# Optimization experiments

Hardware: AMD Instinct MI355X
Metric: run time of the kernel (lower is better)

The kernel has to match this reference:

```python
import jax, jax.numpy as jnp
import numpy as np

N = 100000
E = 1600000
F = 128
COMP_RATIO = 4
K = max(1, N // COMP_RATIO)


def mean_agg(x, src, tgt, n):
    # mean over in-neighbors: h_i = mean_{(j->i) in edges} x_j
    s = jax.ops.segment_sum(x[src], tgt, num_segments=n)          # [N, F]
    cnt = jax.ops.segment_sum(jnp.ones(src.shape[0], x.dtype), tgt, num_segments=n)
    return s / jnp.maximum(cnt, 1.0)[:, None]


def setup_inputs() -> dict:
    key = jax.random.key(0)
    ks = jax.random.split(key, 10)
    sc = 1.0 / np.sqrt(F)
    return {
        "x": jax.random.normal(ks[0], (N, F), jnp.float32),
        "src": jax.random.randint(ks[1], (E,), 0, N, jnp.int32),
        "tgt": jax.random.randint(ks[2], (E,), 0, N, jnp.int32),
        "W_self": jax.random.normal(ks[3], (F, F), jnp.float32) * sc,
        "W_neigh": jax.random.normal(ks[4], (F, F), jnp.float32) * sc,
        "b_pack": jnp.zeros((F,), jnp.float32),
        "w_score": jax.random.normal(ks[5], (F, 1), jnp.float32) * sc,
        "b_score": jnp.zeros((1,), jnp.float32),
        "W_u1": jax.random.normal(ks[6], (F, F), jnp.float32) * sc,
        "b_u1": jnp.zeros((F,), jnp.float32),
        "W_u2": jax.random.normal(ks[7], (F, F), jnp.float32) * sc,
        "b_u2": jnp.zeros((F,), jnp.float32),
    }


def reference(x, src, tgt, W_self, W_neigh, b_pack, w_score, b_score,
              W_u1, b_u1, W_u2, b_u2):
    # ---- compress ----
    # SAGEConv (mean aggregator): fc_self(x) + fc_neigh(mean_neigh(x)) + bias
    h = x @ W_self + mean_agg(x, src, tgt, N) @ W_neigh + b_pack  # [N, F]
    # scorer: Linear(F,1) + Sigmoid
    score = jax.nn.sigmoid(h @ w_score + b_score)[:, 0]           # [N]
    # pool: topk scores, gate selected features by their score
    sel_scores, idx = jax.lax.top_k(score, K)                     # [K], [K]
    new_val = h[idx] * sel_scores[:, None]                        # [K, F]
    # ---- decompress ----
    z = jnp.zeros((N, F), x.dtype).at[idx].set(new_val)
    # diffusion layer 1 (SageConvExt update_func='diffuse'):
    # propagate neighbor mean, keep the received (seed) features fixed
    d = mean_agg(z, src, tgt, N) @ W_u1 + b_u1
    d = d.at[idx].set(z[idx])
    d = jax.nn.relu(d)
    # diffusion layer 2
    out = mean_agg(d, src, tgt, N) @ W_u2 + b_u2
    out = out.at[idx].set(d[idx])
    return out
```

## Files before the change

### kernel.cpp

```cpp
#include <hip/hip_runtime.h>

#define NN 100000
#define NE 1600000
#define FF 128
#define KK 25000
#define NB ((NN + 255) / 256)
#define BM 64
#define BK 32
#define GEMM_GRID ((NN + BM - 1) / BM)

#define BKT_SHIFT 11
#define NPBK (1 << BKT_SHIFT)
#define NBKT2 ((NN + NPBK - 1) >> BKT_SHIFT)
#define NBLKA 512
#define CHUNKA ((NE + NBLKA - 1) / NBLKA)

__device__ __forceinline__ unsigned short f2b(float f) {
  unsigned u = __float_as_uint(f);
  u += 0x7FFFu + ((u >> 16) & 1u);
  return (unsigned short)(u >> 16);
}
__device__ __forceinline__ unsigned pack2(float lo, float hi) {
  return (unsigned)f2b(lo) | ((unsigned)f2b(hi) << 16);
}

__device__ __forceinline__ unsigned long long topk_key(float s, unsigned i) {
  return (((unsigned long long)__float_as_uint(s)) << 32) |
         (unsigned long long)(0xFFFFFFFFu - i);
}

__global__ __launch_bounds__(256) void k_histA(const int* __restrict__ tgt,
                                               int* __restrict__ histg) {
  __shared__ int h[NBKT2];
  for (int i = threadIdx.x; i < NBKT2; i += 256) h[i] = 0;
  __syncthreads();
  int b = blockIdx.x;
  int e0 = b * CHUNKA, e1 = min(e0 + CHUNKA, NE);
  for (int e = e0 + threadIdx.x; e < e1; e += 256)
    atomicAdd(&h[tgt[e] >> BKT_SHIFT], 1);
  __syncthreads();
  for (int i = threadIdx.x; i < NBKT2; i += 256) histg[i * NBLKA + b] = h[i];
}

__global__ __launch_bounds__(1024) void k_scanA(int* __restrict__ histg,
                                                int* __restrict__ bbase) {
  const int M = NBKT2 * NBLKA;
  const int C = (M + 1023) / 1024;
  __shared__ int part[1024];
  __shared__ int tmp[1024];
  int t = threadIdx.x;
  int i0 = t * C;
  int iend = min(i0 + C, M);
  int s = 0;
  for (int i = i0; i < iend; ++i) s += histg[i];
  part[t] = s;
  __syncthreads();
  int* A = part;
  int* B = tmp;
  for (int off = 1; off < 1024; off <<= 1) {
    int v = A[t] + (t >= off ? A[t - off] : 0);
    B[t] = v;
    __syncthreads();
    int* sw = A; A = B; B = sw;
  }
  int run = (t > 0) ? A[t - 1] : 0;
  for (int i = i0; i < iend; ++i) {
    int v = histg[i];
    histg[i] = run;
    run += v;
  }
  __syncthreads();
  if (t < NBKT2) bbase[t] = histg[t * NBLKA];
  if (t == 0) bbase[NBKT2] = NE;
}

__global__ __launch_bounds__(256) void k_scatterA(const int* __restrict__ src,
                                                  const int* __restrict__ tgt,
                                                  const int* __restrict__ histg,
                                                  int2* __restrict__ pairs) {
  __shared__ int cur[NBKT2];
  int b = blockIdx.x;
  for (int i = threadIdx.x; i < NBKT2; i += 256) cur[i] = histg[i * NBLKA + b];
  __syncthreads();
  int e0 = b * CHUNKA, e1 = min(e0 + CHUNKA, NE);
  for (int e = e0 + threadIdx.x; e < e1; e += 256) {
    int t = tgt[e];
    int p = atomicAdd(&cur[t >> BKT_SHIFT], 1);
    pairs[p] = make_int2(t, src[e]);
  }
}

__global__ __launch_bounds__(1024) void k_bucketB(const int2* __restrict__ pairs,
                                                  const int* __restrict__ bbase,
                                                  int* __restrict__ offsets,
                                                  int* __restrict__ csr) {
  __shared__ int cnt[NPBK];
  __shared__ int part[1024];
  __shared__ int tmp[1024];
  int b = blockIdx.x;
  int t = threadIdx.x;
  int lo = b << BKT_SHIFT;
  int nloc = min(NPBK, NN - lo);
  int base = bbase[b];
  int cntE = bbase[b + 1] - base;
  cnt[t] = 0;
  cnt[t + 1024] = 0;
  __syncthreads();
  for (int p = t; p < cntE; p += 1024)
    atomicAdd(&cnt[pairs[base + p].x - lo], 1);
  __syncthreads();
  int a0 = cnt[2 * t];
  int a1 = cnt[2 * t + 1];
  part[t] = a0 + a1;
  __syncthreads();
  int* A = part;
  int* B = tmp;
  for (int off = 1; off < 1024; off <<= 1) {
    int v = A[t] + (t >= off ? A[t - off] : 0);
    B[t] = v;
    __syncthreads();
    int* sw = A; A = B; B = sw;
  }
  int o0 = (t > 0) ? A[t - 1] : 0;
  int o1 = o0 + a0;
  if (2 * t < nloc) offsets[lo + 2 * t] = base + o0;
  if (2 * t + 1 < nloc) offsets[lo + 2 * t + 1] = base + o1;
  __syncthreads();
  cnt[2 * t] = o0;
  cnt[2 * t + 1] = o1;
  __syncthreads();
  for (int p = t; p < cntE; p += 1024) {
    int2 ts = pairs[base + p];
    int l = ts.x - lo;
    int pos = atomicAdd(&cnt[l], 1);
    csr[base + pos] = ts.y;
  }
  if (b == NBKT2 - 1 && t == 0) offsets[NN] = NE;
}

__global__ __launch_bounds__(256) void k_agg(const float* __restrict__ vals,
                                             const int* __restrict__ csr,
                                             const int* __restrict__ offsets,
                                             float* __restrict__ outv) {
  int w = threadIdx.x >> 6;
  int lane = threadIdx.x & 63;
  int half = lane >> 5;
  int li = lane & 31;
  int node = blockIdx.x * 4 + w;
  if (node >= NN) return;
  int beg = offsets[node];
  int end = offsets[node + 1];
  int deg = end - beg;
  float a0 = 0.f, a1 = 0.f, a2 = 0.f, a3 = 0.f;
  int e = beg;
  int e8 = beg + (deg & ~7);
  for (; e < e8; e += 8) {
    float4 v[4];
#pragma unroll
    for (int q = 0; q < 4; ++q) {
      int j = csr[e + 2 * q + half];
      v[q] = *reinterpret_cast<const float4*>(&vals[(size_t)j * FF + li * 4]);
    }
#pragma unroll
    for (int q = 0; q < 4; ++q) {
      a0 += v[q].x; a1 += v[q].y; a2 += v[q].z; a3 += v[q].w;
    }
  }
  for (; e + 2 <= end; e += 2) {
    int j = csr[e + half];
    float4 v = *reinterpret_cast<const float4*>(&vals[(size_t)j * FF + li * 4]);
    a0 += v.x; a1 += v.y; a2 += v.z; a3 += v.w;
  }
  if (e < end && half == 0) {
    int j = csr[e];
    float4 v = *reinterpret_cast<const float4*>(&vals[(size_t)j * FF + li * 4]);
    a0 += v.x; a1 += v.y; a2 += v.z; a3 += v.w;
  }
  a0 += __shfl_xor(a0, 32, 64);
  a1 += __shfl_xor(a1, 32, 64);
  a2 += __shfl_xor(a2, 32, 64);
  a3 += __shfl_xor(a3, 32, 64);
  if (half == 0) {
    float inv = 1.0f / (float)(deg > 0 ? deg : 1);
    *reinterpret_cast<float4*>(&outv[(size_t)node * FF + li * 4]) =
        make_float4(a0 * inv, a1 * inv, a2 * inv, a3 * inv);
  }
}

template <bool GATED>
__global__ __launch_bounds__(256) void k_agg_bf(const unsigned* __restrict__ vals,
                                                const int* __restrict__ csr,
                                                const int* __restrict__ offsets,
                                                const float* __restrict__ sel,
                                                unsigned* __restrict__ outv) {
  int w = threadIdx.x >> 6;
  int lane = threadIdx.x & 63;
  int half = lane >> 5;
  int li = lane & 31;
  int node = blockIdx.x * 4 + w;
  if (node >= NN) return;
  int beg = offsets[node];
  int end = offsets[node + 1];
  int deg = end - beg;
  float a0 = 0.f, a1 = 0.f, a2 = 0.f, a3 = 0.f;
  int e = beg;
  int e8 = beg + (deg & ~7);
  for (; e < e8; e += 8) {
    uint2 u[4];
#pragma unroll
    for (int q = 0; q < 4; ++q) {
      int j = csr[e + 2 * q + half];
      u[q] = (!GATED || sel[j] != 0.f)
                 ? *reinterpret_cast<const uint2*>(&vals[(size_t)j * (FF / 2) + li * 2])
                 : make_uint2(0u, 0u);
    }
#pragma unroll
    for (int q = 0; q < 4; ++q) {
      a0 += __uint_as_float(u[q].x << 16);
      a1 += __uint_as_float(u[q].x & 0xFFFF0000u);
      a2 += __uint_as_float(u[q].y << 16);
      a3 += __uint_as_float(u[q].y & 0xFFFF0000u);
    }
  }
  for (; e + 2 <= end; e += 2) {
    int j = csr[e + half];
    uint2 u = (!GATED || sel[j] != 0.f)
                  ? *reinterpret_cast<const uint2*>(&vals[(size_t)j * (FF / 2) + li * 2])
                  : make_uint2(0u, 0u);
    a0 += __uint_as_float(u.x << 16);
    a1 += __uint_as_float(u.x & 0xFFFF0000u);
    a2 += __uint_as_float(u.y << 16);
    a3 += __uint_as_float(u.y & 0xFFFF0000u);
  }
  if (e < end && half == 0) {
    int j = csr[e];
    uint2 u = (!GATED || sel[j] != 0.f)
                  ? *reinterpret_cast<const uint2*>(&vals[(size_t)j * (FF / 2) + li * 2])
                  : make_uint2(0u, 0u);
    a0 += __uint_as_float(u.x << 16);
    a1 += __uint_as_float(u.x & 0xFFFF0000u);
    a2 += __uint_as_float(u.y << 16);
    a3 += __uint_as_float(u.y & 0xFFFF0000u);
  }
  a0 += __shfl_xor(a0, 32, 64);
  a1 += __shfl_xor(a1, 32, 64);
  a2 += __shfl_xor(a2, 32, 64);
  a3 += __shfl_xor(a3, 32, 64);
  if (half == 0) {
    float inv = 1.0f / (float)(deg > 0 ? deg : 1);
    uint2 o;
    o.x = pack2(a0 * inv, a1 * inv);
    o.y = pack2(a2 * inv, a3 * inv);
    *reinterpret_cast<uint2*>(&outv[(size_t)node * (FF / 2) + li * 2]) = o;
  }
}

template <int EPI, bool DUAL, bool ABF16>
__global__ __launch_bounds__(256) void k_gemm4(const void* __restrict__ Araw,
                                               const float* __restrict__ W,
                                               const float* __restrict__ A2,
                                               const float* __restrict__ W2,
                                               const float* __restrict__ bias,
                                               const float* __restrict__ aux,
                                               const float* __restrict__ score,
                                               const float* __restrict__ sel,
                                               float* __restrict__ outv,
                                               unsigned* __restrict__ obf,
                                               const float* __restrict__ wsc,
                                               const float* __restrict__ bsc,
                                               float* __restrict__ score_out) {
  __shared__ float As[BK][BM + 4];
  __shared__ float Ws[BK][FF];
  const int tid = threadIdx.x;
  const int tx = tid & 15;
  const int ty = tid >> 4;
  const int m0 = blockIdx.x * BM;

  float acc[4][8];
#pragma unroll
  for (int r = 0; r < 4; ++r)
#pragma unroll
    for (int j = 0; j < 8; ++j) acc[r][j] = 0.f;

  const int NPASS = DUAL ? 2 : 1;
  for (int pass = 0; pass < NPASS; ++pass) {
    const float* Wp = (pass == 0) ? W : W2;
    for (int kt = 0; kt < FF; kt += BK) {
      __syncthreads();
      if (pass == 0 && ABF16) {
        const unsigned* Ab = (const unsigned*)Araw;
#pragma unroll
        for (int t = 0; t < 4; ++t) {
          int i = tid + t * 256;
          int row = i >> 4;
          int cu = i & 15;
          int gr = m0 + row;
          unsigned u = (gr < NN) ? Ab[(size_t)gr * (FF / 2) + (kt >> 1) + cu] : 0u;
          As[cu * 2 + 0][row] = __uint_as_float(u << 16);
          As[cu * 2 + 1][row] = __uint_as_float(u & 0xFFFF0000u);
        }
      } else {
        const float* Ag = (pass == 0) ? (const float*)Araw : A2;
#pragma unroll
        for (int t = 0; t < 2; ++t) {
          int i = tid + t * 256;
          int row = i >> 3;
          int c8 = i & 7;
          int gr = m0 + row;
          float4 v = make_float4(0.f, 0.f, 0.f, 0.f);
          if (gr < NN) v = *(const float4*)&Ag[(size_t)gr * FF + kt + c8 * 4];
          As[c8 * 4 + 0][row] = v.x;
          As[c8 * 4 + 1][row] = v.y;
          As[c8 * 4 + 2][row] = v.z;
          As[c8 * 4 + 3][row] = v.w;
        }
      }
#pragma unroll
      for (int t = 0; t < 4; ++t) {
        int i = tid + t * 256;
        int kr = i >> 5;
        int c4 = i & 31;
        *(float4*)&Ws[kr][c4 * 4] =
            *(const float4*)&Wp[(size_t)(kt + kr) * FF + c4 * 4];
      }
      __syncthreads();
#pragma unroll
      for (int k = 0; k < BK; ++k) {
        float4 a = *(const float4*)&As[k][ty * 4];
        float4 w0 = *(const float4*)&Ws[k][tx * 4];
        float4 w1 = *(const float4*)&Ws[k][tx * 4 + 64];
        float av[4] = {a.x, a.y, a.z, a.w};
        float wv[8] = {w0.x, w0.y, w0.z, w0.w, w1.x, w1.y, w1.z, w1.w};
#pragma unroll
        for (int r = 0; r < 4; ++r)
#pragma unroll
          for (int j = 0; j < 8; ++j) acc[r][j] = fmaf(av[r], wv[j], acc[r][j]);
      }
    }
  }

  float4 b0 = *(const float4*)&bias[tx * 4];
  float4 b1 = *(const float4*)&bias[tx * 4 + 64];
  float bs[8] = {b0.x, b0.y, b0.z, b0.w, b1.x, b1.y, b1.z, b1.w};

  if constexpr (EPI == 0) {
    __shared__ float sp[BM][17];
    float4 s0 = *(const float4*)&wsc[tx * 4];
    float4 s1 = *(const float4*)&wsc[tx * 4 + 64];
    float sv[8] = {s0.x, s0.y, s0.z, s0.w, s1.x, s1.y, s1.z, s1.w};
#pragma unroll
    for (int r = 0; r < 4; ++r) {
      int gi = m0 + ty * 4 + r;
      if (gi >= NN) continue;
      size_t base = (size_t)gi * FF;
      float v[8];
      float p = 0.f;
#pragma unroll
      for (int j = 0; j < 8; ++j) {
        v[j] = acc[r][j] + bs[j];
        p = fmaf(v[j], sv[j], p);
      }
      sp[ty * 4 + r][tx] = p;
      *(float4*)&outv[base + tx * 4] = make_float4(v[0], v[1], v[2], v[3]);
      *(float4*)&outv[base + tx * 4 + 64] = make_float4(v[4], v[5], v[6], v[7]);
    }
    __syncthreads();
    if (tid < BM) {
      int gi = m0 + tid;
      if (gi < NN) {
        float s = 0.f;
#pragma unroll
        for (int t = 0; t < 16; ++t) s += sp[tid][t];
        float z = s + bsc[0];
        score_out[gi] = 1.0f / (1.0f + expf(-z));
      }
    }
  } else {
#pragma unroll
    for (int r = 0; r < 4; ++r) {
      int gi = m0 + ty * 4 + r;
      if (gi >= NN) continue;
      size_t base = (size_t)gi * FF;
      float se = sel[gi];
      if (EPI == 1) {
        float v[8];
        if (se != 0.f) {
          float sc = score[gi];
          float4 x0 = *(const float4*)&aux[base + tx * 4];
          float4 x1 = *(const float4*)&aux[base + tx * 4 + 64];
          float av[8] = {x0.x, x0.y, x0.z, x0.w, x1.x, x1.y, x1.z, x1.w};
#pragma unroll
          for (int j = 0; j < 8; ++j) v[j] = fmaxf(av[j] * sc, 0.f);
          *(float4*)&outv[base + tx * 4] = make_float4(v[0], v[1], v[2], v[3]);
          *(float4*)&outv[base + tx * 4 + 64] = make_float4(v[4], v[5], v[6], v[7]);
        } else {
#pragma unroll
          for (int j = 0; j < 8; ++j) v[j] = fmaxf(acc[r][j] + bs[j], 0.f);
        }
        uint2 p0, p1;
        p0.x = pack2(v[0], v[1]);
        p0.y = pack2(v[2], v[3]);
        p1.x = pack2(v[4], v[5]);
        p1.y = pack2(v[6], v[7]);
        *(uint2*)&obf[(size_t)gi * (FF / 2) + tx * 2] = p0;
        *(uint2*)&obf[(size_t)gi * (FF / 2) + 32 + tx * 2] = p1;
      } else {
        float v[8];
        if (se != 0.f) {
          float4 x0 = *(const float4*)&aux[base + tx * 4];
          float4 x1 = *(const float4*)&aux[base + tx * 4 + 64];
          v[0] = x0.x; v[1] = x0.y; v[2] = x0.z; v[3] = x0.w;
          v[4] = x1.x; v[5] = x1.y; v[6] = x1.z; v[7] = x1.w;
        } else {
#pragma unroll
          for (int j = 0; j < 8; ++j) v[j] = acc[r][j] + bs[j];
        }
        *(float4*)&outv[base + tx * 4] = make_float4(v[0], v[1], v[2], v[3]);
        *(float4*)&outv[base + tx * 4 + 64] = make_float4(v[4], v[5], v[6], v[7]);
      }
    }
  }
}

__global__ void k_init_state(unsigned* state) {
  state[0] = 0u;
  state[1] = 0u;
  state[2] = KK;
}

__global__ __launch_bounds__(256) void k_hist(const float* __restrict__ score,
                                              const unsigned* __restrict__ state,
                                              unsigned* __restrict__ hist,
                                              int bits_fixed) {
  __shared__ unsigned lh[256];
  for (int i = threadIdx.x; i < 256; i += 256) lh[i] = 0;
  __syncthreads();
  unsigned long long prefix =
      (((unsigned long long)state[0]) << 32) | (unsigned long long)state[1];
  int i = blockIdx.x * 256 + threadIdx.x;
  if (i < NN) {
    unsigned long long key = topk_key(score[i], (unsigned)i);
    bool ok = (bits_fixed == 0) ? true : (((key ^ prefix) >> (64 - bits_fixed)) == 0ull);
    if (ok) {
      unsigned b = (unsigned)((key >> (56 - bits_fixed)) & 0xFFull);
      atomicAdd(&lh[b], 1u);
    }
  }
  __syncthreads();
  for (int i2 = threadIdx.x; i2 < 256; i2 += 256)
    if (lh[i2]) atomicAdd(&hist[i2], lh[i2]);
}

__global__ __launch_bounds__(256) void k_select_round(unsigned* __restrict__ state,
                                                      unsigned* __restrict__ hist,
                                                      int bits_fixed) {
  __shared__ unsigned h[256];
  int t = threadIdx.x;
  h[t] = hist[t];
  hist[t] = 0;
  __syncthreads();
  if (t == 0) {
    unsigned rem = state[2];
    unsigned long long prefix =
        (((unsigned long long)state[0]) << 32) | (unsigned long long)state[1];
    unsigned cum = 0;
    int bstar = 0;
    for (int b = 255; b >= 0; --b) {
      unsigned c = h[b];
      if (cum + c >= rem) { bstar = b; break; }
      cum += c;
    }
    rem -= cum;
    prefix |= ((unsigned long long)bstar) << (56 - bits_fixed);
    state[0] = (unsigned)(prefix >> 32);
    state[1] = (unsigned)(prefix & 0xFFFFFFFFull);
    state[2] = rem;
  }
}

__global__ __launch_bounds__(256) void k_gate_zg(const float* __restrict__ h,
                                                 const float* __restrict__ score,
                                                 const unsigned* __restrict__ state,
                                                 float* __restrict__ sel,
                                                 unsigned* __restrict__ zg) {
  int w = threadIdx.x >> 6;
  int lane = threadIdx.x & 63;
  int node = blockIdx.x * 4 + w;
  if (node >= NN) return;
  unsigned long long T =
      (((unsigned long long)state[0]) << 32) | (unsigned long long)state[1];
  float s = score[node];
  bool selected = topk_key(s, (unsigned)node) >= T;
  if (lane == 0) sel[node] = selected ? 1.0f : 0.0f;
  if (!selected) return;
  float2 v = *reinterpret_cast<const float2*>(&h[(size_t)node * FF + lane * 2]);
  zg[(size_t)node * (FF / 2) + lane] = pack2(v.x * s, v.y * s);
}

extern "C" void kernel_launch(void* const* d_in, const int* in_sizes, int n_in,
                              void* d_out, int out_size, void* d_ws, size_t ws_size,
                              hipStream_t stream) {
  const float* x = (const float*)d_in[0];
  const int* src = (const int*)d_in[1];
  const int* tgt = (const int*)d_in[2];
  const float* W_self = (const float*)d_in[3];
  const float* W_neigh = (const float*)d_in[4];
  const float* b_pack = (const float*)d_in[5];
  const float* w_score = (const float*)d_in[6];
  const float* b_score = (const float*)d_in[7];
  const float* W_u1 = (const float*)d_in[8];
  const float* b_u1 = (const float*)d_in[9];
  const float* W_u2 = (const float*)d_in[10];
  const float* b_u2 = (const float*)d_in[11];
  float* out = (float*)d_out;

  char* ws = (char*)d_ws;
  size_t off = 0;
  auto alloc = [&](size_t bytes) -> char* {
    char* p = ws + off;
    off += (bytes + 255) & ~(size_t)255;
    return p;
  };
  int* offsets = (int*)alloc((size_t)(NN + 1) * 4);
  int* csr = (int*)alloc((size_t)NE * 4);
  int* histg = (int*)alloc((size_t)NBKT2 * NBLKA * 4);
  int* bbase = (int*)alloc((size_t)(NBKT2 + 1) * 4);
  float* score = (float*)alloc((size_t)NN * 4);
  float* sel = (float*)alloc((size_t)NN * 4);
  unsigned* hist = (unsigned*)alloc(256 * 4);
  unsigned* state = (unsigned*)alloc(64);
  float* aggF = (float*)alloc((size_t)NN * FF * 4);
  int2* pairs = (int2*)aggF;
  unsigned* zdbf = (unsigned*)aggF;
  unsigned* aggBF = (unsigned*)(aggF + (size_t)NN * (FF / 2));
  float* bufB = out;

  hipMemsetAsync(hist, 0, 256 * 4, stream);
  k_init_state<<<1, 1, 0, stream>>>(state);

  k_histA<<<NBLKA, 256, 0, stream>>>(tgt, histg);
  k_scanA<<<1, 1024, 0, stream>>>(histg, bbase);
  k_scatterA<<<NBLKA, 256, 0, stream>>>(src, tgt, histg, pairs);
  k_bucketB<<<NBKT2, 1024, 0, stream>>>(pairs, bbase, offsets, csr);

  k_agg<<<NN / 4, 256, 0, stream>>>(x, csr, offsets, aggF);
  k_gemm4<0, true, false><<<GEMM_GRID, 256, 0, stream>>>(
      aggF, W_neigh, x, W_self, b_pack, nullptr, nullptr, nullptr, bufB, nullptr,
      w_score, b_score, score);

  for (int r = 0; r < 8; ++r) {
    k_hist<<<NB, 256, 0, stream>>>(score, state, hist, 8 * r);
    k_select_round<<<1, 256, 0, stream>>>(state, hist, 8 * r);
  }

  k_gate_zg<<<NN / 4, 256, 0, stream>>>(bufB, score, state, sel, zdbf);
  k_agg_bf<true><<<NN / 4, 256, 0, stream>>>(zdbf, csr, offsets, sel, aggBF);
  k_gemm4<1, false, true><<<GEMM_GRID, 256, 0, stream>>>(
      aggBF, W_u1, nullptr, nullptr, b_u1, bufB, score, sel, bufB, zdbf,
      nullptr, nullptr, nullptr);
  k_agg_bf<false><<<NN / 4, 256, 0, stream>>>(zdbf, csr, offsets, nullptr, aggBF);
  k_gemm4<2, false, true><<<GEMM_GRID, 256, 0, stream>>>(
      aggBF, W_u2, nullptr, nullptr, b_u2, bufB, nullptr, sel, out, nullptr,
      nullptr, nullptr, nullptr);
}
```

Measured before the change: 646.0 us.

## Replace 8-round radix top-k with two 16-bit passes and explicit tie-break

The top-k threshold search moves from eight 8-bit radix rounds over 64-bit score/index keys to two 16-bit histogram passes over the float bits. Ties at the threshold are then resolved by index order using a block count, a scan and a final select kernel that writes the selection mask. A separate kernel also precomputes a masked CSR so the gated aggregation skips the per-edge sel lookup. The aim is to cut the number of tiny serial launches and the dependent sel gather, at the cost of extra 64K-entry histograms, larger memsets and one more pass over the edge list.

```diff
diff --git a/kernel.cpp b/kernel.cpp
--- a/kernel.cpp
+++ b/kernel.cpp
@@ -22,11 +22,6 @@
 }
 __device__ __forceinline__ unsigned pack2(float lo, float hi) {
   return (unsigned)f2b(lo) | ((unsigned)f2b(hi) << 16);
-}
-
-__device__ __forceinline__ unsigned long long topk_key(float s, unsigned i) {
-  return (((unsigned long long)__float_as_uint(s)) << 32) |
-         (unsigned long long)(0xFFFFFFFFu - i);
 }
 
 __global__ __launch_bounds__(256) void k_histA(const int* __restrict__ tgt,
@@ -191,7 +186,6 @@
 __global__ __launch_bounds__(256) void k_agg_bf(const unsigned* __restrict__ vals,
                                                 const int* __restrict__ csr,
                                                 const int* __restrict__ offsets,
-                                                const float* __restrict__ sel,
                                                 unsigned* __restrict__ outv) {
   int w = threadIdx.x >> 6;
   int lane = threadIdx.x & 63;
@@ -210,7 +204,7 @@
 #pragma unroll
     for (int q = 0; q < 4; ++q) {
       int j = csr[e + 2 * q + half];
-      u[q] = (!GATED || sel[j] != 0.f)
+      u[q] = (!GATED || j >= 0)
                  ? *reinterpret_cast<const uint2*>(&vals[(size_t)j * (FF / 2) + li * 2])
                  : make_uint2(0u, 0u);
     }
@@ -224,7 +218,7 @@
   }
   for (; e + 2 <= end; e += 2) {
     int j = csr[e + half];
-    uint2 u = (!GATED || sel[j] != 0.f)
+    uint2 u = (!GATED || j >= 0)
                   ? *reinterpret_cast<const uint2*>(&vals[(size_t)j * (FF / 2) + li * 2])
                   : make_uint2(0u, 0u);
     a0 += __uint_as_float(u.x << 16);
@@ -234,7 +228,7 @@
   }
   if (e < end && half == 0) {
     int j = csr[e];
-    uint2 u = (!GATED || sel[j] != 0.f)
+    uint2 u = (!GATED || j >= 0)
                   ? *reinterpret_cast<const uint2*>(&vals[(size_t)j * (FF / 2) + li * 2])
                   : make_uint2(0u, 0u);
     a0 += __uint_as_float(u.x << 16);
@@ -428,73 +422,142 @@
   state[2] = KK;
 }
 
-__global__ __launch_bounds__(256) void k_hist(const float* __restrict__ score,
-                                              const unsigned* __restrict__ state,
-                                              unsigned* __restrict__ hist,
-                                              int bits_fixed) {
-  __shared__ unsigned lh[256];
-  for (int i = threadIdx.x; i < 256; i += 256) lh[i] = 0;
-  __syncthreads();
-  unsigned long long prefix =
-      (((unsigned long long)state[0]) << 32) | (unsigned long long)state[1];
+template <int PHASE>
+__global__ __launch_bounds__(256) void k_h16(const float* __restrict__ score,
+                                             const unsigned* __restrict__ state,
+                                             int* __restrict__ hist) {
   int i = blockIdx.x * 256 + threadIdx.x;
+  if (i >= NN) return;
+  unsigned bits = __float_as_uint(score[i]);
+  if (PHASE == 0) {
+    atomicAdd(&hist[bits >> 16], 1);
+  } else {
+    if ((bits >> 16) == state[0]) atomicAdd(&hist[bits & 0xFFFFu], 1);
+  }
+}
+
+template <int PHASE>
+__global__ __launch_bounds__(1024) void k_sel16(const int* __restrict__ hist,
+                                                unsigned* __restrict__ state) {
+  __shared__ int part[1024];
+  __shared__ int tmp[1024];
+  int t = threadIdx.x;
+  int base = t * 64;
+  int lsum = 0;
+  for (int b = 0; b < 64; ++b) lsum += hist[base + b];
+  part[t] = lsum;
+  __syncthreads();
+  int* A = part;
+  int* B = tmp;
+  for (int off = 1; off < 1024; off <<= 1) {
+    int v = A[t] + (t >= off ? A[t - off] : 0);
+    B[t] = v;
+    __syncthreads();
+    int* sw = A; A = B; B = sw;
+  }
+  int total = A[1023];
+  int incl = A[t];
+  unsigned rem = state[2];
+  int running = total - incl;
+  for (int b = 63; b >= 0; --b) {
+    int c = hist[base + b];
+    if ((unsigned)running < rem && rem <= (unsigned)(running + c)) {
+      if (PHASE == 0) state[0] = (unsigned)(base + b);
+      else state[1] = (unsigned)(base + b);
+      state[2] = rem - (unsigned)running;
+    }
+    running += c;
+  }
+}
+
+__global__ __launch_bounds__(256) void k_eqcount(const float* __restrict__ score,
+                                                 const unsigned* __restrict__ state,
+                                                 int* __restrict__ eqc) {
+  __shared__ int s[256];
+  int i = blockIdx.x * 256 + threadIdx.x;
+  unsigned T = (state[0] << 16) | state[1];
+  int eq = (i < NN && __float_as_uint(score[i]) == T) ? 1 : 0;
+  s[threadIdx.x] = eq;
+  __syncthreads();
+  for (int off = 128; off > 0; off >>= 1) {
+    if (threadIdx.x < off) s[threadIdx.x] += s[threadIdx.x + off];
+    __syncthreads();
+  }
+  if (threadIdx.x == 0) eqc[blockIdx.x] = s[0];
+}
+
+__global__ __launch_bounds__(512) void k_eqscan(const int* __restrict__ eqc,
+                                                int* __restrict__ eqoff) {
+  __shared__ int s[512];
+  __shared__ int tmp[512];
+  int t = threadIdx.x;
+  int own = (t < NB) ? eqc[t] : 0;
+  s[t] = own;
+  __syncthreads();
+  int* A = s;
+  int* B = tmp;
+  for (int off = 1; off < 512; off <<= 1) {
+    int v = A[t] + (t >= off ? A[t - off] : 0);
+    B[t] = v;
+    __syncthreads();
+    int* sw = A; A = B; B = sw;
+  }
+  if (t < NB) eqoff[t] = A[t] - own;
+}
+
+__global__ __launch_bounds__(256) void k_tb(const float* __restrict__ score,
+                                            const unsigned* __restrict__ state,
+                                            const int* __restrict__ eqoff,
+                                            float* __restrict__ sel) {
+  __shared__ int s[256];
+  __shared__ int tmp[256];
+  int blk = blockIdx.x;
+  int i = blk * 256 + threadIdx.x;
+  unsigned T = (state[0] << 16) | state[1];
+  unsigned rem = state[2];
+  unsigned bits = (i < NN) ? __float_as_uint(score[i]) : 0u;
+  int eq = (i < NN && bits == T) ? 1 : 0;
+  s[threadIdx.x] = eq;
+  __syncthreads();
+  int* A = s;
+  int* B = tmp;
+  for (int off = 1; off < 256; off <<= 1) {
+    int v = A[threadIdx.x] + (threadIdx.x >= off ? A[threadIdx.x - off] : 0);
+    B[threadIdx.x] = v;
+    __syncthreads();
+    int* sw = A; A = B; B = sw;
+  }
+  int excl = A[threadIdx.x] - eq;
   if (i < NN) {
-    unsigned long long key = topk_key(score[i], (unsigned)i);
-    bool ok = (bits_fixed == 0) ? true : (((key ^ prefix) >> (64 - bits_fixed)) == 0ull);
-    if (ok) {
-      unsigned b = (unsigned)((key >> (56 - bits_fixed)) & 0xFFull);
-      atomicAdd(&lh[b], 1u);
-    }
-  }
-  __syncthreads();
-  for (int i2 = threadIdx.x; i2 < 256; i2 += 256)
-    if (lh[i2]) atomicAdd(&hist[i2], lh[i2]);
-}
-
-__global__ __launch_bounds__(256) void k_select_round(unsigned* __restrict__ state,
-                                                      unsigned* __restrict__ hist,
-                                                      int bits_fixed) {
-  __shared__ unsigned h[256];
-  int t = threadIdx.x;
-  h[t] = hist[t];
-  hist[t] = 0;
-  __syncthreads();
-  if (t == 0) {
-    unsigned rem = state[2];
-    unsigned long long prefix =
-        (((unsigned long long)state[0]) << 32) | (unsigned long long)state[1];
-    unsigned cum = 0;
-    int bstar = 0;
-    for (int b = 255; b >= 0; --b) {
-      unsigned c = h[b];
-      if (cum + c >= rem) { bstar = b; break; }
-      cum += c;
-    }
-    rem -= cum;
-    prefix |= ((unsigned long long)bstar) << (56 - bits_fixed);
-    state[0] = (unsigned)(prefix >> 32);
-    state[1] = (unsigned)(prefix & 0xFFFFFFFFull);
-    state[2] = rem;
+    float sv = 0.f;
+    if (bits > T) sv = 1.f;
+    else if (eq && (unsigned)(eqoff[blk] + excl) < rem) sv = 1.f;
+    sel[i] = sv;
   }
 }
 
 __global__ __launch_bounds__(256) void k_gate_zg(const float* __restrict__ h,
                                                  const float* __restrict__ score,
-                                                 const unsigned* __restrict__ state,
-                                                 float* __restrict__ sel,
+                                                 const float* __restrict__ sel,
                                                  unsigned* __restrict__ zg) {
   int w = threadIdx.x >> 6;
   int lane = threadIdx.x & 63;
   int node = blockIdx.x * 4 + w;
   if (node >= NN) return;
-  unsigned long long T =
-      (((unsigned long long)state[0]) << 32) | (unsigned long long)state[1];
+  if (sel[node] == 0.f) return;
   float s = score[node];
-  bool selected = topk_key(s, (unsigned)node) >= T;
-  if (lane == 0) sel[node] = selected ? 1.0f : 0.0f;
-  if (!selected) return;
   float2 v = *reinterpret_cast<const float2*>(&h[(size_t)node * FF + lane * 2]);
   zg[(size_t)node * (FF / 2) + lane] = pack2(v.x * s, v.y * s);
+}
+
+__global__ __launch_bounds__(256) void k_mask_csr(const int* __restrict__ csr,
+                                                  const float* __restrict__ sel,
+                                                  int* __restrict__ csr2) {
+  int e = blockIdx.x * 256 + threadIdx.x;
+  if (e < NE) {
+    int j = csr[e];
+    csr2[e] = (sel[j] != 0.f) ? j : -1;
+  }
 }
 
 extern "C" void kernel_launch(void* const* d_in, const int* in_sizes, int n_in,
@@ -523,19 +586,24 @@
   };
   int* offsets = (int*)alloc((size_t)(NN + 1) * 4);
   int* csr = (int*)alloc((size_t)NE * 4);
+  int* csr2 = (int*)alloc((size_t)NE * 4);
   int* histg = (int*)alloc((size_t)NBKT2 * NBLKA * 4);
   int* bbase = (int*)alloc((size_t)(NBKT2 + 1) * 4);
   float* score = (float*)alloc((size_t)NN * 4);
   float* sel = (float*)alloc((size_t)NN * 4);
-  unsigned* hist = (unsigned*)alloc(256 * 4);
+  int* hist0 = (int*)alloc(65536 * 4);
+  int* hist1 = (int*)alloc(65536 * 4);
   unsigned* state = (unsigned*)alloc(64);
+  int* eqc = (int*)alloc((size_t)NB * 4);
+  int* eqoff = (int*)alloc((size_t)NB * 4);
   float* aggF = (float*)alloc((size_t)NN * FF * 4);
   int2* pairs = (int2*)aggF;
   unsigned* zdbf = (unsigned*)aggF;
   unsigned* aggBF = (unsigned*)(aggF + (size_t)NN * (FF / 2));
   float* bufB = out;
 
-  hipMemsetAsync(hist, 0, 256 * 4, stream);
+  hipMemsetAsync(hist0, 0, 65536 * 4, stream);
+  hipMemsetAsync(hist1, 0, 65536 * 4, stream);
   k_init_state<<<1, 1, 0, stream>>>(state);
 
   k_histA<<<NBLKA, 256, 0, stream>>>(tgt, histg);
@@ -548,17 +616,21 @@
       aggF, W_neigh, x, W_self, b_pack, nullptr, nullptr, nullptr, bufB, nullptr,
       w_score, b_score, score);
 
-  for (int r = 0; r < 8; ++r) {
-    k_hist<<<NB, 256, 0, stream>>>(score, state, hist, 8 * r);
-    k_select_round<<<1, 256, 0, stream>>>(state, hist, 8 * r);
-  }
-
-  k_gate_zg<<<NN / 4, 256, 0, stream>>>(bufB, score, state, sel, zdbf);
-  k_agg_bf<true><<<NN / 4, 256, 0, stream>>>(zdbf, csr, offsets, sel, aggBF);
+  k_h16<0><<<NB, 256, 0, stream>>>(score, state, hist0);
+  k_sel16<0><<<1, 1024, 0, stream>>>(hist0, state);
+  k_h16<1><<<NB, 256, 0, stream>>>(score, state, hist1);
+  k_sel16<1><<<1, 1024, 0, stream>>>(hist1, state);
+  k_eqcount<<<NB, 256, 0, stream>>>(score, state, eqc);
+  k_eqscan<<<1, 512, 0, stream>>>(eqc, eqoff);
+  k_tb<<<NB, 256, 0, stream>>>(score, state, eqoff, sel);
+
+  k_gate_zg<<<NN / 4, 256, 0, stream>>>(bufB, score, sel, zdbf);
+  k_mask_csr<<<(NE + 255) / 256, 256, 0, stream>>>(csr, sel, csr2);
+  k_agg_bf<true><<<NN / 4, 256, 0, stream>>>(zdbf, csr2, offsets, aggBF);
   k_gemm4<1, false, true><<<GEMM_GRID, 256, 0, stream>>>(
       aggBF, W_u1, nullptr, nullptr, b_u1, bufB, score, sel, bufB, zdbf,
       nullptr, nullptr, nullptr);
-  k_agg_bf<false><<<NN / 4, 256, 0, stream>>>(zdbf, csr, offsets, nullptr, aggBF);
+  k_agg_bf<false><<<NN / 4, 256, 0, stream>>>(zdbf, csr, offsets, aggBF);
   k_gemm4<2, false, true><<<GEMM_GRID, 256, 0, stream>>>(
       aggBF, W_u2, nullptr, nullptr, b_u2, bufB, nullptr, sel, out, nullptr,
       nullptr, nullptr, nullptr);
```

Result: slower. 684.6 us (+6.0%).
